# Performance work log

Hardware: AMD Instinct MI355X
Metric: run time of the kernel (lower is better)

Reference implementation:

```python
import jax, jax.numpy as jnp
import numpy as np

D_MODEL = 1024
N_HEAD = 16
DK = D_MODEL // N_HEAD
D_FF = 2048
EPS = 1e-6
NEG = -1e10


def layer_norm(x, gamma, beta):
    # torch .std() is unbiased (N-1), and eps is added to std (not var)
    mean = jnp.mean(x, axis=-1, keepdims=True)
    var = jnp.sum((x - mean) ** 2, axis=-1, keepdims=True) / (x.shape[-1] - 1)
    std = jnp.sqrt(var)
    return gamma * (x - mean) / (std + EPS) + beta


def setup_inputs() -> dict:
    key = jax.random.key(0)
    ks = jax.random.split(key, 12)
    s = 0.02
    inp = {
        'x': jax.random.normal(ks[0], (16, 512, D_MODEL), dtype=jnp.float32),
        'x_mask': jax.random.randint(ks[1], (16, 1, 1, 512), 0, 2, dtype=jnp.int32),
        'Wq': jax.random.normal(ks[2], (D_MODEL, D_MODEL), dtype=jnp.float32) * s,
        'bq': jnp.zeros((D_MODEL,), jnp.float32),
        'Wk': jax.random.normal(ks[3], (D_MODEL, D_MODEL), dtype=jnp.float32) * s,
        'bk': jnp.zeros((D_MODEL,), jnp.float32),
        'Wv': jax.random.normal(ks[4], (D_MODEL, D_MODEL), dtype=jnp.float32) * s,
        'bv': jnp.zeros((D_MODEL,), jnp.float32),
        'Wo': jax.random.normal(ks[5], (D_MODEL, D_MODEL), dtype=jnp.float32) * s,
        'bo': jnp.zeros((D_MODEL,), jnp.float32),
        'gamma1': jnp.ones((D_MODEL,), jnp.float32),
        'beta1': jnp.zeros((D_MODEL,), jnp.float32),
        'W1': jax.random.normal(ks[6], (D_MODEL, D_FF), dtype=jnp.float32) * s,
        'b1': jnp.zeros((D_FF,), jnp.float32),
        'W2': jax.random.normal(ks[7], (D_FF, D_MODEL), dtype=jnp.float32) * s,
        'b2': jnp.zeros((D_MODEL,), jnp.float32),
        'gamma2': jnp.ones((D_MODEL,), jnp.float32),
        'beta2': jnp.zeros((D_MODEL,), jnp.float32),
    }
    return inp


def reference(x, x_mask, Wq, bq, Wk, bk, Wv, bv, Wo, bo, gamma1, beta1,
              W1, b1, W2, b2, gamma2, beta2):
    B, S, _ = x.shape
    # QKV projections -> [B, S, H, DK]
    q = (x @ Wq + bq).reshape(B, S, N_HEAD, DK)
    k = (x @ Wk + bk).reshape(B, S, N_HEAD, DK)
    v = (x @ Wv + bv).reshape(B, S, N_HEAD, DK)
    # scores [B, H, Sq, Sk]
    scores = jnp.einsum('bqhd,bkhd->bhqk', q, k) / jnp.sqrt(jnp.float32(DK))
    scores = jnp.where(x_mask == 0, jnp.float32(NEG), scores)
    probs = jax.nn.softmax(scores, axis=-1)
    attn = jnp.einsum('bhqk,bkhd->bqhd', probs, v).reshape(B, S, D_MODEL)
    attn_out = attn @ Wo + bo
    # residual + post-LN 1
    h = layer_norm(attn_out + x, gamma1, beta1)
    # FFN (exact GELU as torch nn.GELU default)
    ffn = jax.nn.gelu(h @ W1 + b1, approximate=False) @ W2 + b2
    out = layer_norm(ffn + h, gamma2, beta2)
    return out
```

## Files before the change

kernel.cpp:

```cpp
#include <hip/hip_runtime.h>
#include <math.h>

#define B_ 16
#define S_ 512
#define DM 1024
#define NH 16
#define DFF 2048

typedef short bf16x8 __attribute__((ext_vector_type(8)));
typedef float f32x4 __attribute__((ext_vector_type(4)));
typedef unsigned short u16;

__device__ __forceinline__ u16 f2bf(float f) {
  unsigned int u = __float_as_uint(f);
  u += 0x7FFF + ((u >> 16) & 1);
  return (u16)(u >> 16);
}

__device__ __forceinline__ float gelu_exact(float x) {
  return 0.5f * x * (1.0f + erff(x * 0.70710678118654752f));
}

__device__ __forceinline__ void gload_lds16(const void* g, void* l) {
  __builtin_amdgcn_global_load_lds((const __attribute__((address_space(1))) void*)g,
                                   (__attribute__((address_space(3))) void*)l, 16, 0, 0);
}


__global__ void cvt_bf16_k(const float* __restrict__ in, u16* __restrict__ out, int n) {
  int i = (blockIdx.x * blockDim.x + threadIdx.x) * 4;
  float4 v = *(const float4*)(in + i);
  uint2 pk;
  pk.x = (unsigned)f2bf(v.x) | ((unsigned)f2bf(v.y) << 16);
  pk.y = (unsigned)f2bf(v.z) | ((unsigned)f2bf(v.w) << 16);
  *(uint2*)(out + i) = pk;
}

__global__ void transpose_bf16(const float* __restrict__ W, u16* __restrict__ Wt, int K, int N) {
  __shared__ float tile[32][33];
  int n0 = blockIdx.x * 32, k0 = blockIdx.y * 32;
  int tx = threadIdx.x, ty = threadIdx.y;
#pragma unroll
  for (int j = 0; j < 32; j += 8)
    tile[ty + j][tx] = W[(size_t)(k0 + ty + j) * N + n0 + tx];
  __syncthreads();
#pragma unroll
  for (int j = 0; j < 32; j += 8)
    Wt[(size_t)(n0 + ty + j) * K + k0 + tx] = f2bf(tile[tx][ty + j]);
}

__global__ void bias_cat(const float* __restrict__ bq, const float* __restrict__ bk,
                         const float* __restrict__ bv, float* __restrict__ o) {
  int i = blockIdx.x * 256 + threadIdx.x;
  o[i] = (i < 1024) ? bq[i] : ((i < 2048) ? bk[i - 1024] : bv[i - 2048]);
}

template <int EPI>
__global__ __launch_bounds__(256, 3)
void gemm128(const u16* __restrict__ A, const u16* __restrict__ Bt,
             const float* __restrict__ bias, void* __restrict__ Cout,
             u16* __restrict__ vT, int M, int N, int K) {
  __shared__ __align__(16) char lds[49152];
  const int tid = threadIdx.x;
  const int w = tid >> 6, lane = tid & 63;
  const int wm = w >> 1, wn = w & 1;

  const int gx = gridDim.x;
  const int nwg = gx * gridDim.y;
  const int lin = blockIdx.y * gx + blockIdx.x;
  const int wg = (lin & 7) * (nwg >> 3) + (lin >> 3);
  const int bm = wg / gx, bn = wg % gx;

  const int NT = K >> 5;

  const int srow = tid >> 2;
  const int scol = ((tid & 3) * 8) ^ (((tid >> 5) & 1) * 16);
  const u16* gA = A + (size_t)(bm * 128 + srow) * K + scol;
  const u16* gB = Bt + (size_t)(bn * 128 + srow) * K + scol;
  const size_t rstep = (size_t)64 * K;
  char* const ldsA = lds;
  char* const ldsB = lds + 8192;
  const int dstbase = w * 1024;

  const int lr = lane & 15;
  const int kph = ((lane >> 4) * 16) ^ ((lane & 8) ? 32 : 0);
  const char* const fA = ldsA + (wm * 64 + lr) * 64 + kph;
  const char* const fB = ldsB + (wn * 64 + lr) * 64 + kph;

  f32x4 acc[4][4];
#pragma unroll
  for (int i = 0; i < 4; ++i)
#pragma unroll
    for (int j = 0; j < 4; ++j) acc[i][j] = (f32x4){0.f, 0.f, 0.f, 0.f};

#pragma unroll
  for (int pt = 0; pt < 2; ++pt) {
    const u16* ga = gA + pt * 32;
    const u16* gb = gB + pt * 32;
    const int so = pt * 16384;
    gload_lds16(ga, ldsA + so + dstbase);
    gload_lds16(ga + rstep, ldsA + so + 4096 + dstbase);
    gload_lds16(gb, ldsB + so + dstbase);
    gload_lds16(gb + rstep, ldsB + so + 4096 + dstbase);
  }
  asm volatile("s_waitcnt vmcnt(4)" ::: "memory");
  __builtin_amdgcn_s_barrier();
  __builtin_amdgcn_sched_barrier(0);

  int cs = 0, ss = 2;
  for (int t = 0; t < NT; ++t) {
    const char* fAc = fA + cs * 16384;
    const char* fBc = fB + cs * 16384;
    bf16x8 af[4], bf[4];
#pragma unroll
    for (int mi = 0; mi < 4; ++mi) af[mi] = *(const bf16x8*)(fAc + mi * 1024);
#pragma unroll
    for (int ni = 0; ni < 4; ++ni) bf[ni] = *(const bf16x8*)(fBc + ni * 1024);
    {
      const int st = (t + 2 < NT) ? (t + 2) : (NT - 1);
      const u16* ga = gA + st * 32;
      const u16* gb = gB + st * 32;
      const int so = ss * 16384;
      gload_lds16(ga, ldsA + so + dstbase);
      gload_lds16(ga + rstep, ldsA + so + 4096 + dstbase);
      gload_lds16(gb, ldsB + so + dstbase);
      gload_lds16(gb + rstep, ldsB + so + 4096 + dstbase);
    }
    asm volatile("s_waitcnt lgkmcnt(0)" ::: "memory");
    __builtin_amdgcn_sched_barrier(0);
    __builtin_amdgcn_s_setprio(1);
#pragma unroll
    for (int mi = 0; mi < 4; ++mi)
#pragma unroll
      for (int ni = 0; ni < 4; ++ni)
        acc[mi][ni] = __builtin_amdgcn_mfma_f32_16x16x32_bf16(af[mi], bf[ni], acc[mi][ni], 0, 0, 0);
    __builtin_amdgcn_s_setprio(0);
    asm volatile("s_waitcnt vmcnt(4)" ::: "memory");
    __builtin_amdgcn_s_barrier();
    __builtin_amdgcn_sched_barrier(0);
    cs = (cs == 2) ? 0 : cs + 1;
    ss = (ss == 2) ? 0 : ss + 1;
  }

  const int crow0 = bm * 128 + wm * 64;
  const int ccol0 = bn * 128 + wn * 64;
#pragma unroll
  for (int mi = 0; mi < 4; ++mi) {
#pragma unroll
    for (int ni = 0; ni < 4; ++ni) {
      const int col = ccol0 + ni * 16 + lr;
      const float bv = bias[col];
#pragma unroll
      for (int r = 0; r < 4; ++r) {
        const int row = crow0 + mi * 16 + (lane >> 4) * 4 + r;
        float v = acc[mi][ni][r] + bv;
        if (EPI == 1) {
          v = gelu_exact(v);
          ((u16*)Cout)[(size_t)row * N + col] = f2bf(v);
        } else if (EPI == 2) {
          ((float*)Cout)[(size_t)row * N + col] = v;
        } else {
          if (col < 2048) {
            ((u16*)Cout)[(size_t)row * 2048 + col] = f2bf(v);
          } else {
            const int b = row >> 9, s = row & 511;
            const int hd = col - 2048;
            vT[((size_t)(b * NH + (hd >> 6)) * 64 + (hd & 63)) * S_ + s] = f2bf(v);
          }
        }
      }
    }
  }
}

__global__ __launch_bounds__(256, 3)
void attn_kernel(const u16* __restrict__ qk,
                 const u16* __restrict__ vT,
                 const int* __restrict__ mask,
                 u16* __restrict__ out) {
  __shared__ __align__(16) u16 Qs[32 * 72];
  __shared__ __align__(16) u16 Pl[32 * 520];
  __shared__ int Ml[512];
  __shared__ __align__(16) float Rmax[32][4];
  __shared__ __align__(16) float Rsum[32][4];

  const int tid = threadIdx.x;
  const int w = tid >> 6, lane = tid & 63;
  const int bid = blockIdx.x;
  const int widx = (bid & 7) * 512 + (bid >> 3);
  const int qt = widx & 15, h = (widx >> 4) & 15, b = widx >> 8;
  const int q0 = qt * 32;
  const int arow = lane & 15, kg = lane >> 4;

  {
    int r = tid >> 3, slot = tid & 7;
    bf16x8 v = *(const bf16x8*)(qk + (size_t)(b * S_ + q0 + r) * 2048 + h * 64 + slot * 8);
    *(bf16x8*)((char*)Qs + r * 144 + slot * 16) = v;
  }
  Ml[tid] = mask[b * S_ + tid];
  Ml[tid + 256] = mask[b * S_ + tid + 256];
  __syncthreads();

  f32x4 s0[8], s1[8];
  {
    bf16x8 af[2][2];
#pragma unroll
    for (int mi = 0; mi < 2; ++mi)
#pragma unroll
      for (int kk = 0; kk < 2; ++kk)
        af[mi][kk] = *(const bf16x8*)((char*)Qs + (mi * 16 + arow) * 144 + kk * 64 + kg * 16);
    const u16* kbase = qk + (size_t)(b * S_) * 2048 + 1024 + h * 64;
#pragma unroll
    for (int ni = 0; ni < 8; ++ni) {
      const int colg = w * 128 + ni * 16 + arow;
      const u16* kr = kbase + (size_t)colg * 2048 + kg * 8;
      bf16x8 bk0 = *(const bf16x8*)(kr);
      bf16x8 bk1 = *(const bf16x8*)(kr + 32);
      f32x4 a0 = {0.f, 0.f, 0.f, 0.f}, a1 = {0.f, 0.f, 0.f, 0.f};
      a0 = __builtin_amdgcn_mfma_f32_16x16x32_bf16(af[0][0], bk0, a0, 0, 0, 0);
      a0 = __builtin_amdgcn_mfma_f32_16x16x32_bf16(af[0][1], bk1, a0, 0, 0, 0);
      a1 = __builtin_amdgcn_mfma_f32_16x16x32_bf16(af[1][0], bk0, a1, 0, 0, 0);
      a1 = __builtin_amdgcn_mfma_f32_16x16x32_bf16(af[1][1], bk1, a1, 0, 0, 0);
      const bool msk = (Ml[colg] == 0);
#pragma unroll
      for (int r = 0; r < 4; ++r) {
        s0[ni][r] = msk ? -1e10f : a0[r] * 0.125f;
        s1[ni][r] = msk ? -1e10f : a1[r] * 0.125f;
      }
    }
  }

  float m0[4], m1[4];
#pragma unroll
  for (int r = 0; r < 4; ++r) {
    float a = fmaxf(fmaxf(s0[0][r], s0[1][r]), fmaxf(s0[2][r], s0[3][r]));
    float c = fmaxf(fmaxf(s0[4][r], s0[5][r]), fmaxf(s0[6][r], s0[7][r]));
    m0[r] = fmaxf(a, c);
    a = fmaxf(fmaxf(s1[0][r], s1[1][r]), fmaxf(s1[2][r], s1[3][r]));
    c = fmaxf(fmaxf(s1[4][r], s1[5][r]), fmaxf(s1[6][r], s1[7][r]));
    m1[r] = fmaxf(a, c);
  }
#pragma unroll
  for (int d = 1; d < 16; d <<= 1) {
#pragma unroll
    for (int r = 0; r < 4; ++r) {
      m0[r] = fmaxf(m0[r], __shfl_xor(m0[r], d));
      m1[r] = fmaxf(m1[r], __shfl_xor(m1[r], d));
    }
  }
  if (arow == 0) {
#pragma unroll
    for (int r = 0; r < 4; ++r) {
      Rmax[kg * 4 + r][w] = m0[r];
      Rmax[16 + kg * 4 + r][w] = m1[r];
    }
  }
  __syncthreads();
  float fm0[4], fm1[4];
#pragma unroll
  for (int r = 0; r < 4; ++r) {
    f32x4 v = *(const f32x4*)&Rmax[kg * 4 + r][0];
    fm0[r] = fmaxf(fmaxf(v[0], v[1]), fmaxf(v[2], v[3]));
    v = *(const f32x4*)&Rmax[16 + kg * 4 + r][0];
    fm1[r] = fmaxf(fmaxf(v[0], v[1]), fmaxf(v[2], v[3]));
  }

  float t0[4] = {0.f, 0.f, 0.f, 0.f}, t1[4] = {0.f, 0.f, 0.f, 0.f};
#pragma unroll
  for (int ni = 0; ni < 8; ++ni) {
#pragma unroll
    for (int r = 0; r < 4; ++r) {
      s0[ni][r] = __expf(s0[ni][r] - fm0[r]);
      t0[r] += s0[ni][r];
      s1[ni][r] = __expf(s1[ni][r] - fm1[r]);
      t1[r] += s1[ni][r];
    }
  }
#pragma unroll
  for (int ni = 0; ni < 8; ++ni) {
    const int colg = w * 128 + ni * 16 + arow;
#pragma unroll
    for (int r = 0; r < 4; ++r) {
      Pl[(kg * 4 + r) * 520 + colg] = f2bf(s0[ni][r]);
      Pl[(16 + kg * 4 + r) * 520 + colg] = f2bf(s1[ni][r]);
    }
  }
#pragma unroll
  for (int d = 1; d < 16; d <<= 1) {
#pragma unroll
    for (int r = 0; r < 4; ++r) {
      t0[r] += __shfl_xor(t0[r], d);
      t1[r] += __shfl_xor(t1[r], d);
    }
  }
  if (arow == 0) {
#pragma unroll
    for (int r = 0; r < 4; ++r) {
      Rsum[kg * 4 + r][w] = t0[r];
      Rsum[16 + kg * 4 + r][w] = t1[r];
    }
  }
  __syncthreads();

  {
    f32x4 oa[2];
    oa[0] = (f32x4){0.f, 0.f, 0.f, 0.f};
    oa[1] = (f32x4){0.f, 0.f, 0.f, 0.f};
    const u16* vb = vT + ((size_t)(b * NH + h) * 64 + w * 16 + arow) * S_ + kg * 8;
#pragma unroll
    for (int t16 = 0; t16 < 16; ++t16) {
      const int sk0 = t16 * 32;
      bf16x8 bfr = *(const bf16x8*)(vb + sk0);
#pragma unroll
      for (int mi = 0; mi < 2; ++mi) {
        bf16x8 pa = *(const bf16x8*)(Pl + (mi * 16 + arow) * 520 + sk0 + kg * 8);
        oa[mi] = __builtin_amdgcn_mfma_f32_16x16x32_bf16(pa, bfr, oa[mi], 0, 0, 0);
      }
    }
#pragma unroll
    for (int mi = 0; mi < 2; ++mi)
#pragma unroll
      for (int r = 0; r < 4; ++r) {
        const int rloc = mi * 16 + kg * 4 + r;
        f32x4 sv = *(const f32x4*)&Rsum[rloc][0];
        const float inv = 1.0f / (sv[0] + sv[1] + sv[2] + sv[3]);
        const int qrow = q0 + rloc;
        out[(size_t)(b * S_ + qrow) * DM + h * 64 + w * 16 + arow] = f2bf(oa[mi][r] * inv);
      }
  }
}

__global__ __launch_bounds__(256)
void ln_kernel(const float* __restrict__ a, const float* __restrict__ res,
               const float* __restrict__ gamma, const float* __restrict__ beta,
               float* __restrict__ out, u16* __restrict__ outb) {
  const int row = blockIdx.x, tid = threadIdx.x;
  const int w = tid >> 6, lane = tid & 63;
  const size_t base = (size_t)row * DM + tid * 4;
  float4 va = *(const float4*)(a + base);
  float4 vr = *(const float4*)(res + base);
  float v0 = va.x + vr.x, v1 = va.y + vr.y, v2 = va.z + vr.z, v3 = va.w + vr.w;
  float s = v0 + v1 + v2 + v3;
  float ss = v0 * v0 + v1 * v1 + v2 * v2 + v3 * v3;
#pragma unroll
  for (int off = 32; off >= 1; off >>= 1) {
    s += __shfl_down(s, off);
    ss += __shfl_down(ss, off);
  }
  __shared__ float ps[4], pss[4], mb[2];
  if (lane == 0) { ps[w] = s; pss[w] = ss; }
  __syncthreads();
  if (tid == 0) {
    float S = ps[0] + ps[1] + ps[2] + ps[3];
    float SS = pss[0] + pss[1] + pss[2] + pss[3];
    float mean = S * (1.0f / DM);
    float var = (SS - (float)DM * mean * mean) * (1.0f / (DM - 1));
    var = fmaxf(var, 0.f);
    mb[0] = mean;
    mb[1] = 1.0f / (sqrtf(var) + 1e-6f);
  }
  __syncthreads();
  const float mean = mb[0], rinv = mb[1];
  const int c = tid * 4;
  float y0 = gamma[c] * (v0 - mean) * rinv + beta[c];
  float y1 = gamma[c + 1] * (v1 - mean) * rinv + beta[c + 1];
  float y2 = gamma[c + 2] * (v2 - mean) * rinv + beta[c + 2];
  float y3 = gamma[c + 3] * (v3 - mean) * rinv + beta[c + 3];
  float4 o = {y0, y1, y2, y3};
  *(float4*)(out + base) = o;
  if (outb) {
    uint2 pk;
    pk.x = (unsigned)f2bf(y0) | ((unsigned)f2bf(y1) << 16);
    pk.y = (unsigned)f2bf(y2) | ((unsigned)f2bf(y3) << 16);
    *(uint2*)(outb + base) = pk;
  }
}


extern "C" void kernel_launch(void* const* d_in, const int* in_sizes, int n_in,
                              void* d_out, int out_size, void* d_ws, size_t ws_size,
                              hipStream_t stream) {
  const float* x = (const float*)d_in[0];
  const int* xm = (const int*)d_in[1];
  const float* Wq = (const float*)d_in[2];
  const float* bq = (const float*)d_in[3];
  const float* Wk = (const float*)d_in[4];
  const float* bk = (const float*)d_in[5];
  const float* Wv = (const float*)d_in[6];
  const float* bv = (const float*)d_in[7];
  const float* Wo = (const float*)d_in[8];
  const float* bo = (const float*)d_in[9];
  const float* g1 = (const float*)d_in[10];
  const float* be1 = (const float*)d_in[11];
  const float* W1 = (const float*)d_in[12];
  const float* b1 = (const float*)d_in[13];
  const float* W2 = (const float*)d_in[14];
  const float* b2 = (const float*)d_in[15];
  const float* g2 = (const float*)d_in[16];
  const float* be2 = (const float*)d_in[17];

  char* ws = (char*)d_ws;
  u16* xb = (u16*)(ws);
  u16* wqkvt = (u16*)(ws + 16777216);
  u16* wot = (u16*)(ws + 23068672);
  u16* w1t = (u16*)(ws + 25165824);
  u16* w2t = (u16*)(ws + 29360128);
  float* bqkv = (float*)(ws + 33554432);
  u16* qkb = (u16*)(ws + 33566720);
  u16* vtb = (u16*)(ws + 67121152);
  u16* attnb = (u16*)(ws + 83898368);
  float* f32a = (float*)(ws + 100675584);
  float* hbuf = (float*)(ws + 134230016);
  u16* hb = xb;

  cvt_bf16_k<<<dim3(8192), dim3(256), 0, stream>>>(x, xb, 8388608);
  transpose_bf16<<<dim3(32, 32), dim3(32, 8), 0, stream>>>(Wq, wqkvt, 1024, 1024);
  transpose_bf16<<<dim3(32, 32), dim3(32, 8), 0, stream>>>(Wk, wqkvt + 1024 * 1024, 1024, 1024);
  transpose_bf16<<<dim3(32, 32), dim3(32, 8), 0, stream>>>(Wv, wqkvt + 2 * 1024 * 1024, 1024, 1024);
  transpose_bf16<<<dim3(32, 32), dim3(32, 8), 0, stream>>>(Wo, wot, 1024, 1024);
  transpose_bf16<<<dim3(64, 32), dim3(32, 8), 0, stream>>>(W1, w1t, 1024, 2048);
  transpose_bf16<<<dim3(32, 64), dim3(32, 8), 0, stream>>>(W2, w2t, 2048, 1024);
  bias_cat<<<dim3(12), dim3(256), 0, stream>>>(bq, bk, bv, bqkv);

  gemm128<3><<<dim3(24, 64), dim3(256), 0, stream>>>(xb, wqkvt, bqkv, (void*)qkb, vtb, 8192, 3072, 1024);
  attn_kernel<<<dim3(4096), dim3(256), 0, stream>>>(qkb, vtb, xm, attnb);
  gemm128<2><<<dim3(8, 64), dim3(256), 0, stream>>>(attnb, wot, bo, (void*)f32a, (u16*)nullptr, 8192, 1024, 1024);
  ln_kernel<<<dim3(8192), dim3(256), 0, stream>>>(f32a, x, g1, be1, hbuf, hb);
  gemm128<1><<<dim3(16, 64), dim3(256), 0, stream>>>(hb, w1t, b1, (void*)qkb, (u16*)nullptr, 8192, 2048, 1024);
  gemm128<2><<<dim3(8, 64), dim3(256), 0, stream>>>(qkb, w2t, b2, (void*)f32a, (u16*)nullptr, 8192, 1024, 2048);
  ln_kernel<<<dim3(8192), dim3(256), 0, stream>>>(f32a, hbuf, g2, be2, (float*)d_out, (u16*)nullptr);
}
```

Measured before the change: 343.5 us.

## Deepen GEMM pipeline to four LDS stages with register double-buffered fragments

The GEMM main loop goes from three LDS buffers with a prefetch distance of two to four buffers with a prefetch distance of three. The loop is unrolled by two so A/B fragments are ping-ponged between register sets, and the next tile's LDS reads are issued before the current tile's MFMAs, which hides LDS latency behind compute. The epilogue also packs four consecutive bf16 V-transpose values into one vector store instead of four scalar stores. The cost is 64KB of LDS per block instead of 48KB, which lowers how many blocks fit per CU below the launch-bounds target of three, plus extra fragment registers.

```diff
diff --git a/kernel.cpp b/kernel.cpp
--- a/kernel.cpp
+++ b/kernel.cpp
@@ -60,7 +60,7 @@
 void gemm128(const u16* __restrict__ A, const u16* __restrict__ Bt,
              const float* __restrict__ bias, void* __restrict__ Cout,
              u16* __restrict__ vT, int M, int N, int K) {
-  __shared__ __align__(16) char lds[49152];
+  __shared__ __align__(16) char lds[65536];
   const int tid = threadIdx.x;
   const int w = tid >> 6, lane = tid & 63;
   const int wm = w >> 1, wn = w & 1;
@@ -93,54 +93,83 @@
 #pragma unroll
     for (int j = 0; j < 4; ++j) acc[i][j] = (f32x4){0.f, 0.f, 0.f, 0.f};
 
-#pragma unroll
-  for (int pt = 0; pt < 2; ++pt) {
-    const u16* ga = gA + pt * 32;
-    const u16* gb = gB + pt * 32;
-    const int so = pt * 16384;
-    gload_lds16(ga, ldsA + so + dstbase);
-    gload_lds16(ga + rstep, ldsA + so + 4096 + dstbase);
-    gload_lds16(gb, ldsB + so + dstbase);
-    gload_lds16(gb + rstep, ldsB + so + 4096 + dstbase);
-  }
+#define STAGE_TILE(st_, slot_)                                     \
+  do {                                                             \
+    const u16* ga_ = gA + (st_) * 32;                              \
+    const u16* gb_ = gB + (st_) * 32;                              \
+    const int so_ = (slot_) * 16384;                               \
+    gload_lds16(ga_, ldsA + so_ + dstbase);                        \
+    gload_lds16(ga_ + rstep, ldsA + so_ + 4096 + dstbase);         \
+    gload_lds16(gb_, ldsB + so_ + dstbase);                        \
+    gload_lds16(gb_ + rstep, ldsB + so_ + 4096 + dstbase);         \
+  } while (0)
+
+  STAGE_TILE(0, 0);
+  STAGE_TILE(1, 1);
+  STAGE_TILE(2, 2);
   asm volatile("s_waitcnt vmcnt(4)" ::: "memory");
   __builtin_amdgcn_s_barrier();
   __builtin_amdgcn_sched_barrier(0);
 
-  int cs = 0, ss = 2;
-  for (int t = 0; t < NT; ++t) {
-    const char* fAc = fA + cs * 16384;
-    const char* fBc = fB + cs * 16384;
-    bf16x8 af[4], bf[4];
-#pragma unroll
-    for (int mi = 0; mi < 4; ++mi) af[mi] = *(const bf16x8*)(fAc + mi * 1024);
-#pragma unroll
-    for (int ni = 0; ni < 4; ++ni) bf[ni] = *(const bf16x8*)(fBc + ni * 1024);
+  bf16x8 afP[4], bfP[4], afQ[4], bfQ[4];
+  {
+    const char* fAc = fA;
+    const char* fBc = fB;
+#pragma unroll
+    for (int mi = 0; mi < 4; ++mi) afP[mi] = *(const bf16x8*)(fAc + mi * 1024);
+#pragma unroll
+    for (int ni = 0; ni < 4; ++ni) bfP[ni] = *(const bf16x8*)(fBc + ni * 1024);
+  }
+  asm volatile("s_waitcnt lgkmcnt(0)" ::: "memory");
+  __builtin_amdgcn_sched_barrier(0);
+
+  for (int tt = 0; tt < (NT >> 1); ++tt) {
+    const int t = tt * 2;
     {
-      const int st = (t + 2 < NT) ? (t + 2) : (NT - 1);
-      const u16* ga = gA + st * 32;
-      const u16* gb = gB + st * 32;
-      const int so = ss * 16384;
-      gload_lds16(ga, ldsA + so + dstbase);
-      gload_lds16(ga + rstep, ldsA + so + 4096 + dstbase);
-      gload_lds16(gb, ldsB + so + dstbase);
-      gload_lds16(gb + rstep, ldsB + so + 4096 + dstbase);
-    }
-    asm volatile("s_waitcnt lgkmcnt(0)" ::: "memory");
-    __builtin_amdgcn_sched_barrier(0);
-    __builtin_amdgcn_s_setprio(1);
-#pragma unroll
-    for (int mi = 0; mi < 4; ++mi)
-#pragma unroll
-      for (int ni = 0; ni < 4; ++ni)
-        acc[mi][ni] = __builtin_amdgcn_mfma_f32_16x16x32_bf16(af[mi], bf[ni], acc[mi][ni], 0, 0, 0);
-    __builtin_amdgcn_s_setprio(0);
-    asm volatile("s_waitcnt vmcnt(4)" ::: "memory");
-    __builtin_amdgcn_s_barrier();
-    __builtin_amdgcn_sched_barrier(0);
-    cs = (cs == 2) ? 0 : cs + 1;
-    ss = (ss == 2) ? 0 : ss + 1;
-  }
+      const int rs = (t + 1) & 3;
+      const char* fAc = fA + rs * 16384;
+      const char* fBc = fB + rs * 16384;
+#pragma unroll
+      for (int mi = 0; mi < 4; ++mi) afQ[mi] = *(const bf16x8*)(fAc + mi * 1024);
+#pragma unroll
+      for (int ni = 0; ni < 4; ++ni) bfQ[ni] = *(const bf16x8*)(fBc + ni * 1024);
+      const int st = (t + 3 < NT) ? (t + 3) : (NT - 1);
+      STAGE_TILE(st, (t + 3) & 3);
+      __builtin_amdgcn_s_setprio(1);
+#pragma unroll
+      for (int mi = 0; mi < 4; ++mi)
+#pragma unroll
+        for (int ni = 0; ni < 4; ++ni)
+          acc[mi][ni] = __builtin_amdgcn_mfma_f32_16x16x32_bf16(afP[mi], bfP[ni], acc[mi][ni], 0, 0, 0);
+      __builtin_amdgcn_s_setprio(0);
+      asm volatile("s_waitcnt vmcnt(4) lgkmcnt(0)" ::: "memory");
+      __builtin_amdgcn_s_barrier();
+      __builtin_amdgcn_sched_barrier(0);
+    }
+    {
+      const int rt = (t + 2 < NT) ? (t + 2) : (NT - 1);
+      const int rs = rt & 3;
+      const char* fAc = fA + rs * 16384;
+      const char* fBc = fB + rs * 16384;
+#pragma unroll
+      for (int mi = 0; mi < 4; ++mi) afP[mi] = *(const bf16x8*)(fAc + mi * 1024);
+#pragma unroll
+      for (int ni = 0; ni < 4; ++ni) bfP[ni] = *(const bf16x8*)(fBc + ni * 1024);
+      const int st = (t + 4 < NT) ? (t + 4) : (NT - 1);
+      STAGE_TILE(st, (t + 4) & 3);
+      __builtin_amdgcn_s_setprio(1);
+#pragma unroll
+      for (int mi = 0; mi < 4; ++mi)
+#pragma unroll
+        for (int ni = 0; ni < 4; ++ni)
+          acc[mi][ni] = __builtin_amdgcn_mfma_f32_16x16x32_bf16(afQ[mi], bfQ[ni], acc[mi][ni], 0, 0, 0);
+      __builtin_amdgcn_s_setprio(0);
+      asm volatile("s_waitcnt vmcnt(4) lgkmcnt(0)" ::: "memory");
+      __builtin_amdgcn_s_barrier();
+      __builtin_amdgcn_sched_barrier(0);
+    }
+  }
+#undef STAGE_TILE
 
   const int crow0 = bm * 128 + wm * 64;
   const int ccol0 = bn * 128 + wn * 64;
@@ -150,23 +179,29 @@
     for (int ni = 0; ni < 4; ++ni) {
       const int col = ccol0 + ni * 16 + lr;
       const float bv = bias[col];
-#pragma unroll
-      for (int r = 0; r < 4; ++r) {
-        const int row = crow0 + mi * 16 + (lane >> 4) * 4 + r;
-        float v = acc[mi][ni][r] + bv;
-        if (EPI == 1) {
-          v = gelu_exact(v);
-          ((u16*)Cout)[(size_t)row * N + col] = f2bf(v);
-        } else if (EPI == 2) {
-          ((float*)Cout)[(size_t)row * N + col] = v;
+      const int rowb = crow0 + mi * 16 + (lane >> 4) * 4;
+      float v[4];
+#pragma unroll
+      for (int r = 0; r < 4; ++r) v[r] = acc[mi][ni][r] + bv;
+      if (EPI == 1) {
+#pragma unroll
+        for (int r = 0; r < 4; ++r)
+          ((u16*)Cout)[(size_t)(rowb + r) * N + col] = f2bf(gelu_exact(v[r]));
+      } else if (EPI == 2) {
+#pragma unroll
+        for (int r = 0; r < 4; ++r)
+          ((float*)Cout)[(size_t)(rowb + r) * N + col] = v[r];
+      } else {
+        if (col < 2048) {
+#pragma unroll
+          for (int r = 0; r < 4; ++r)
+            ((u16*)Cout)[(size_t)(rowb + r) * 2048 + col] = f2bf(v[r]);
         } else {
-          if (col < 2048) {
-            ((u16*)Cout)[(size_t)row * 2048 + col] = f2bf(v);
-          } else {
-            const int b = row >> 9, s = row & 511;
-            const int hd = col - 2048;
-            vT[((size_t)(b * NH + (hd >> 6)) * 64 + (hd & 63)) * S_ + s] = f2bf(v);
-          }
+          const int b = rowb >> 9, s = rowb & 511;
+          const int hd = col - 2048;
+          ushort4 pk;
+          pk.x = f2bf(v[0]); pk.y = f2bf(v[1]); pk.z = f2bf(v[2]); pk.w = f2bf(v[3]);
+          *(ushort4*)(vT + ((size_t)(b * NH + (hd >> 6)) * 64 + (hd & 63)) * S_ + s) = pk;
         }
       }
     }
```

New measurement: 338.7 us. Within noise of the previous version (-1.4%).
